# Optimization experiments

Hardware: AMD Instinct MI355X
Metric: run time of the kernel (lower is better)

The kernel has to match this reference:

```python
import jax, jax.numpy as jnp
import numpy as np

IN_FEATURES = 2048
OUT_FEATURES = 4096
NUM_SHIFTS = 10  # perms


def setup_inputs() -> dict:
    key = jax.random.key(0)
    kx, kw = jax.random.split(key)
    x = jax.random.normal(kx, (4, 2048, IN_FEATURES), dtype=jnp.float32)
    # nn.Linear weight: (out_features, in_features), Kaiming-uniform-ish init
    bound = 1.0 / np.sqrt(IN_FEATURES)
    W = jax.random.uniform(kw, (OUT_FEATURES, IN_FEATURES), dtype=jnp.float32,
                           minval=-bound, maxval=bound)
    return {"x": x, "W": W}


def _combined_weight(W):
    # Wt: (in, out). Sum of all weight variants; sum_i(x @ W_i) == x @ sum_i(W_i).
    Wt = W.T
    Weff = Wt + jnp.flip(Wt, axis=0) + jnp.flip(Wt, axis=1)
    for i in range(NUM_SHIFTS // 2):
        Weff = Weff + jnp.roll(Wt, shift=i + 1, axis=1)
        Weff = Weff + jnp.roll(Wt, shift=i + 1, axis=0)
    return Weff  # (in, out)


def reference(x, W):
    # reg_out (x @ W.T) + flipped + rolled variants, collapsed into one GEMM
    Weff = _combined_weight(W)
    return jnp.einsum('bsi,io->bso', x, Weff)
```

## Files before the change

### kernel.cpp

```cpp
#include <hip/hip_runtime.h>
#include <hip/hip_bf16.h>
#include <stdint.h>

#define M_DIM 8192
#define K_DIM 2048
#define N_DIM 4096
#define BM 256
#define BN 256
#define BK 64
#define NT (K_DIM / BK)

typedef __attribute__((ext_vector_type(8))) short bf16x8;
typedef __attribute__((ext_vector_type(4))) float f32x4;

__device__ __forceinline__ unsigned short f2bfu(float f) {
    __hip_bfloat16 h = __float2bfloat16(f);
    return __builtin_bit_cast(unsigned short, h);
}

__global__ void build_weff(const float* __restrict__ W, unsigned short* __restrict__ WT) {
    const int o = blockIdx.x;
    const float* wo  = W + (size_t)o * K_DIM;
    const float* wfo = W + (size_t)(N_DIM - 1 - o) * K_DIM;
    const float* wr0 = W + (size_t)((o - 1) & (N_DIM - 1)) * K_DIM;
    const float* wr1 = W + (size_t)((o - 2) & (N_DIM - 1)) * K_DIM;
    const float* wr2 = W + (size_t)((o - 3) & (N_DIM - 1)) * K_DIM;
    const float* wr3 = W + (size_t)((o - 4) & (N_DIM - 1)) * K_DIM;
    const float* wr4 = W + (size_t)((o - 5) & (N_DIM - 1)) * K_DIM;
    for (int i = threadIdx.x; i < K_DIM; i += 256) {
        float acc = wo[i] + wo[K_DIM - 1 - i] + wfo[i];
        acc += wo[(i - 1) & (K_DIM - 1)];
        acc += wo[(i - 2) & (K_DIM - 1)];
        acc += wo[(i - 3) & (K_DIM - 1)];
        acc += wo[(i - 4) & (K_DIM - 1)];
        acc += wo[(i - 5) & (K_DIM - 1)];
        acc += wr0[i] + wr1[i] + wr2[i] + wr3[i] + wr4[i];
        WT[(size_t)o * K_DIM + i] = f2bfu(acc);
    }
}

__global__ void cvt_x_kernel(const float* __restrict__ x, unsigned short* __restrict__ xb) {
    const int idx = blockIdx.x * 256 + threadIdx.x;
    float4 v = ((const float4*)x)[idx];
    ushort4 o;
    o.x = f2bfu(v.x); o.y = f2bfu(v.y); o.z = f2bfu(v.z); o.w = f2bfu(v.w);
    ((ushort4*)xb)[idx] = o;
}

__global__ __launch_bounds__(512, 2) void gemm256(const unsigned short* __restrict__ Ab,
                                                  const unsigned short* __restrict__ Bt,
                                                  float* __restrict__ C) {
    __shared__ __align__(16) char smem[2 * 65536];

    const int tid  = threadIdx.x;
    const int wave = tid >> 6;
    const int lane = tid & 63;

    const int nwg = gridDim.x;
    const int cpx = nwg >> 3;
    const int wg  = (blockIdx.x & 7) * cpx + (blockIdx.x >> 3);
    const int nbn = N_DIM / BN;
    const int bm0 = (wg / nbn) * BM;
    const int bn0 = (wg % nbn) * BN;

    const int wr = wave >> 2;
    const int wc = wave & 3;

    const int srow = wave * 8 + (lane >> 3);
    const int lsw  = (lane & 7) ^ ((lane >> 3) & 7);
    const unsigned short* gA0 = Ab + (size_t)(bm0 + srow) * K_DIM + lsw * 8;
    const unsigned short* gB0 = Bt + (size_t)(bn0 + srow) * K_DIM + lsw * 8;

    const int r16   = lane & 15;
    const int slot0 = (((lane >> 4) | 0) ^ (lane & 7)) * 16;
    const int slot1 = (((lane >> 4) | 4) ^ (lane & 7)) * 16;
    const int aRow  = (wr * 128 + r16) * 128;
    const int bRow  = (wc * 64  + r16) * 128;

    f32x4 acc[8][4] = {};

#define STAGE(kt, p) do {                                                          \
    char* ldsA = smem + (p) * 65536 + wave * 1024;                                 \
    char* ldsB = ldsA + 32768;                                                     \
    const unsigned short* ga = gA0 + (kt) * BK;                                    \
    const unsigned short* gb = gB0 + (kt) * BK;                                    \
    _Pragma("unroll")                                                              \
    for (int j = 0; j < 4; ++j)                                                    \
        __builtin_amdgcn_global_load_lds(                                          \
            (const __attribute__((address_space(1))) unsigned int*)(ga + (size_t)j * 64 * K_DIM), \
            (__attribute__((address_space(3))) unsigned int*)(ldsA + j * 8192),    \
            16, 0, 0);                                                             \
    _Pragma("unroll")                                                              \
    for (int j = 0; j < 4; ++j)                                                    \
        __builtin_amdgcn_global_load_lds(                                          \
            (const __attribute__((address_space(1))) unsigned int*)(gb + (size_t)j * 64 * K_DIM), \
            (__attribute__((address_space(3))) unsigned int*)(ldsB + j * 8192),    \
            16, 0, 0);                                                             \
} while (0)

    STAGE(0, 0);
    STAGE(1, 1);

    for (int k = 0; k < NT; ++k) {
        const int p = k & 1;

        if (k + 1 < NT) asm volatile("s_waitcnt vmcnt(8)" ::: "memory");
        else            asm volatile("s_waitcnt vmcnt(0)" ::: "memory");
        __builtin_amdgcn_s_barrier();
        __builtin_amdgcn_sched_barrier(0);

        const char* bufA = smem + p * 65536;
        const char* bufB = bufA + 32768;

        bf16x8 b[4][2];
#pragma unroll
        for (int fn = 0; fn < 4; ++fn) {
            b[fn][0] = *(const bf16x8*)(bufB + bRow + fn * (16 * 128) + slot0);
            b[fn][1] = *(const bf16x8*)(bufB + bRow + fn * (16 * 128) + slot1);
        }
#pragma unroll
        for (int qm = 0; qm < 2; ++qm) {
            bf16x8 a[4][2];
#pragma unroll
            for (int fm = 0; fm < 4; ++fm) {
                a[fm][0] = *(const bf16x8*)(bufA + aRow + (qm * 64 + fm * 16) * 128 + slot0);
                a[fm][1] = *(const bf16x8*)(bufA + aRow + (qm * 64 + fm * 16) * 128 + slot1);
            }
            __builtin_amdgcn_s_setprio(1);
#pragma unroll
            for (int fm = 0; fm < 4; ++fm)
#pragma unroll
                for (int fn = 0; fn < 4; ++fn) {
                    acc[qm * 4 + fm][fn] = __builtin_amdgcn_mfma_f32_16x16x32_bf16(
                        a[fm][0], b[fn][0], acc[qm * 4 + fm][fn], 0, 0, 0);
                    acc[qm * 4 + fm][fn] = __builtin_amdgcn_mfma_f32_16x16x32_bf16(
                        a[fm][1], b[fn][1], acc[qm * 4 + fm][fn], 0, 0, 0);
                }
            __builtin_amdgcn_s_setprio(0);
        }

        asm volatile("s_waitcnt lgkmcnt(0)" ::: "memory");
        __builtin_amdgcn_sched_barrier(0);
        __builtin_amdgcn_s_barrier();
        __builtin_amdgcn_sched_barrier(0);

        if (k + 2 < NT) STAGE(k + 2, p);
    }
#undef STAGE

    const int crow = (lane >> 4) * 4;
    const int ccol = lane & 15;
    float* Cb = C + (size_t)(bm0 + wr * 128 + crow) * N_DIM + (bn0 + wc * 64 + ccol);
#pragma unroll
    for (int fm = 0; fm < 8; ++fm)
#pragma unroll
        for (int fn = 0; fn < 4; ++fn)
#pragma unroll
            for (int r = 0; r < 4; ++r)
                Cb[(size_t)(fm * 16 + r) * N_DIM + fn * 16] = acc[fm][fn][r];
}

extern "C" void kernel_launch(void* const* d_in, const int* in_sizes, int n_in,
                              void* d_out, int out_size, void* d_ws, size_t ws_size,
                              hipStream_t stream) {
    const float* x = (const float*)d_in[0];
    const float* W = (const float*)d_in[1];
    float* out = (float*)d_out;

    unsigned short* xb = (unsigned short*)d_ws;
    unsigned short* wt = (unsigned short*)((char*)d_ws + (size_t)M_DIM * K_DIM * 2);

    build_weff<<<N_DIM, 256, 0, stream>>>(W, wt);
    cvt_x_kernel<<<(M_DIM * K_DIM) / 4 / 256, 256, 0, stream>>>(x, xb);

    dim3 grid((M_DIM / BM) * (N_DIM / BN));
    gemm256<<<grid, 512, 0, stream>>>(xb, wt, out);
}
```

Before: 186.7 us.

## Split GEMM main loop into eight-phase ping-pong schedule with half-tile prefetch

```diff
diff --git a/kernel.cpp b/kernel.cpp
--- a/kernel.cpp
+++ b/kernel.cpp
@@ -9,6 +9,7 @@
 #define BN 256
 #define BK 64
 #define NT (K_DIM / BK)
+#define NITER (NT / 2)
 
 typedef __attribute__((ext_vector_type(8))) short bf16x8;
 typedef __attribute__((ext_vector_type(4))) float f32x4;
@@ -47,9 +48,9 @@
     ((ushort4*)xb)[idx] = o;
 }
 
-__global__ __launch_bounds__(512, 2) void gemm256(const unsigned short* __restrict__ Ab,
-                                                  const unsigned short* __restrict__ Bt,
-                                                  float* __restrict__ C) {
+__global__ __launch_bounds__(512, 2) void gemm8p(const unsigned short* __restrict__ Ab,
+                                                 const unsigned short* __restrict__ Bt,
+                                                 float* __restrict__ C) {
     __shared__ __align__(16) char smem[2 * 65536];
 
     const int tid  = threadIdx.x;
@@ -66,87 +67,92 @@
     const int wr = wave >> 2;
     const int wc = wave & 3;
 
-    const int srow = wave * 8 + (lane >> 3);
+    const int srow = tid >> 3;
     const int lsw  = (lane & 7) ^ ((lane >> 3) & 7);
     const unsigned short* gA0 = Ab + (size_t)(bm0 + srow) * K_DIM + lsw * 8;
     const unsigned short* gB0 = Bt + (size_t)(bn0 + srow) * K_DIM + lsw * 8;
 
-    const int r16   = lane & 15;
-    const int slot0 = (((lane >> 4) | 0) ^ (lane & 7)) * 16;
-    const int slot1 = (((lane >> 4) | 4) ^ (lane & 7)) * 16;
-    const int aRow  = (wr * 128 + r16) * 128;
-    const int bRow  = (wc * 64  + r16) * 128;
+    const int r16  = lane & 15;
+    const int x7   = lane & 7;
+    const int ksl0 = (((lane >> 4)    ) ^ x7) * 16;
+    const int ksl1 = (((lane >> 4) | 4) ^ x7) * 16;
+    const int aRow = (wr * 128 + r16) * 128;
+    const int bRow = (wc * 64  + r16) * 128 + 32768;
 
-    f32x4 acc[8][4] = {};
+    f32x4  acc[8][4] = {};
+    bf16x8 b[4][2];
 
-#define STAGE(kt, p) do {                                                          \
-    char* ldsA = smem + (p) * 65536 + wave * 1024;                                 \
-    char* ldsB = ldsA + 32768;                                                     \
-    const unsigned short* ga = gA0 + (kt) * BK;                                    \
-    const unsigned short* gb = gB0 + (kt) * BK;                                    \
-    _Pragma("unroll")                                                              \
-    for (int j = 0; j < 4; ++j)                                                    \
-        __builtin_amdgcn_global_load_lds(                                          \
-            (const __attribute__((address_space(1))) unsigned int*)(ga + (size_t)j * 64 * K_DIM), \
-            (__attribute__((address_space(3))) unsigned int*)(ldsA + j * 8192),    \
-            16, 0, 0);                                                             \
-    _Pragma("unroll")                                                              \
-    for (int j = 0; j < 4; ++j)                                                    \
-        __builtin_amdgcn_global_load_lds(                                          \
-            (const __attribute__((address_space(1))) unsigned int*)(gb + (size_t)j * 64 * K_DIM), \
-            (__attribute__((address_space(3))) unsigned int*)(ldsB + j * 8192),    \
-            16, 0, 0);                                                             \
+#define STAGE_HALF(gbase, opoff, h, t, p) do {                                              \
+    char* lds_ = smem + (p) * 65536 + (opoff) + (h) * 16384 + wave * 1024;                  \
+    const unsigned short* g_ = (gbase) + (size_t)((h) * 128) * K_DIM + (t) * BK;            \
+    __builtin_amdgcn_global_load_lds(                                                        \
+        (const __attribute__((address_space(1))) unsigned int*)g_,                           \
+        (__attribute__((address_space(3))) unsigned int*)lds_, 16, 0, 0);                    \
+    __builtin_amdgcn_global_load_lds(                                                        \
+        (const __attribute__((address_space(1))) unsigned int*)(g_ + (size_t)64 * K_DIM),    \
+        (__attribute__((address_space(3))) unsigned int*)(lds_ + 8192), 16, 0, 0);           \
 } while (0)
 
-    STAGE(0, 0);
-    STAGE(1, 1);
+#define PHASE(P, Q, LOADB, STAGE_STMT, VM_STMT) do {                                        \
+    const char* base_ = smem + (P) * 65536;                                                 \
+    bf16x8 a_[2][2];                                                                        \
+    if (LOADB) {                                                                            \
+        _Pragma("unroll")                                                                   \
+        for (int fn = 0; fn < 4; ++fn) {                                                    \
+            b[fn][0] = *(const bf16x8*)(base_ + bRow + fn * 2048 + ksl0);                   \
+            b[fn][1] = *(const bf16x8*)(base_ + bRow + fn * 2048 + ksl1);                   \
+        }                                                                                   \
+    }                                                                                       \
+    a_[0][0] = *(const bf16x8*)(base_ + aRow + (Q) * 4096 + ksl0);                          \
+    a_[0][1] = *(const bf16x8*)(base_ + aRow + (Q) * 4096 + ksl1);                          \
+    a_[1][0] = *(const bf16x8*)(base_ + aRow + (Q) * 4096 + 2048 + ksl0);                   \
+    a_[1][1] = *(const bf16x8*)(base_ + aRow + (Q) * 4096 + 2048 + ksl1);                   \
+    STAGE_STMT;                                                                             \
+    __builtin_amdgcn_s_barrier();                                                           \
+    asm volatile("s_waitcnt lgkmcnt(0)" ::: "memory");                                      \
+    __builtin_amdgcn_sched_barrier(0);                                                      \
+    __builtin_amdgcn_s_setprio(1);                                                          \
+    _Pragma("unroll")                                                                       \
+    for (int fm = 0; fm < 2; ++fm)                                                          \
+        _Pragma("unroll")                                                                   \
+        for (int fn = 0; fn < 4; ++fn) {                                                    \
+            acc[(Q)*2 + fm][fn] = __builtin_amdgcn_mfma_f32_16x16x32_bf16(                  \
+                a_[fm][0], b[fn][0], acc[(Q)*2 + fm][fn], 0, 0, 0);                         \
+            acc[(Q)*2 + fm][fn] = __builtin_amdgcn_mfma_f32_16x16x32_bf16(                  \
+                a_[fm][1], b[fn][1], acc[(Q)*2 + fm][fn], 0, 0, 0);                         \
+        }                                                                                   \
+    __builtin_amdgcn_s_setprio(0);                                                          \
+    VM_STMT;                                                                                \
+    __builtin_amdgcn_s_barrier();                                                           \
+} while (0)
 
-    for (int k = 0; k < NT; ++k) {
-        const int p = k & 1;
+    STAGE_HALF(gA0, 0,     0, 0, 0);
+    STAGE_HALF(gA0, 0,     1, 0, 0);
+    STAGE_HALF(gB0, 32768, 0, 0, 0);
+    STAGE_HALF(gB0, 32768, 1, 0, 0);
+    STAGE_HALF(gB0, 32768, 0, 1, 1);
+    STAGE_HALF(gB0, 32768, 1, 1, 1);
+    asm volatile("s_waitcnt vmcnt(4)" ::: "memory");
+    __builtin_amdgcn_s_barrier();
 
-        if (k + 1 < NT) asm volatile("s_waitcnt vmcnt(8)" ::: "memory");
-        else            asm volatile("s_waitcnt vmcnt(0)" ::: "memory");
-        __builtin_amdgcn_s_barrier();
-        __builtin_amdgcn_sched_barrier(0);
+    for (int u = 0; u < NITER; ++u) {
+        const bool last = (u == NITER - 1);
+        const int  t1 = 2 * u + 1, t2 = 2 * u + 2, t3 = 2 * u + 3;
 
-        const char* bufA = smem + p * 65536;
-        const char* bufB = bufA + 32768;
-
-        bf16x8 b[4][2];
-#pragma unroll
-        for (int fn = 0; fn < 4; ++fn) {
-            b[fn][0] = *(const bf16x8*)(bufB + bRow + fn * (16 * 128) + slot0);
-            b[fn][1] = *(const bf16x8*)(bufB + bRow + fn * (16 * 128) + slot1);
-        }
-#pragma unroll
-        for (int qm = 0; qm < 2; ++qm) {
-            bf16x8 a[4][2];
-#pragma unroll
-            for (int fm = 0; fm < 4; ++fm) {
-                a[fm][0] = *(const bf16x8*)(bufA + aRow + (qm * 64 + fm * 16) * 128 + slot0);
-                a[fm][1] = *(const bf16x8*)(bufA + aRow + (qm * 64 + fm * 16) * 128 + slot1);
-            }
-            __builtin_amdgcn_s_setprio(1);
-#pragma unroll
-            for (int fm = 0; fm < 4; ++fm)
-#pragma unroll
-                for (int fn = 0; fn < 4; ++fn) {
-                    acc[qm * 4 + fm][fn] = __builtin_amdgcn_mfma_f32_16x16x32_bf16(
-                        a[fm][0], b[fn][0], acc[qm * 4 + fm][fn], 0, 0, 0);
-                    acc[qm * 4 + fm][fn] = __builtin_amdgcn_mfma_f32_16x16x32_bf16(
-                        a[fm][1], b[fn][1], acc[qm * 4 + fm][fn], 0, 0, 0);
-                }
-            __builtin_amdgcn_s_setprio(0);
-        }
-
-        asm volatile("s_waitcnt lgkmcnt(0)" ::: "memory");
-        __builtin_amdgcn_sched_barrier(0);
-        __builtin_amdgcn_s_barrier();
-        __builtin_amdgcn_sched_barrier(0);
-
-        if (k + 2 < NT) STAGE(k + 2, p);
+        PHASE(0, 0, 1, { STAGE_HALF(gA0, 0, 0, t1, 1); }, {});
+        PHASE(0, 1, 0, { STAGE_HALF(gA0, 0, 1, t1, 1); }, {});
+        PHASE(0, 2, 0, { if (!last) STAGE_HALF(gB0, 32768, 0, t2, 0); }, {});
+        PHASE(0, 3, 0, { if (!last) STAGE_HALF(gB0, 32768, 1, t2, 0); },
+              { if (last) asm volatile("s_waitcnt vmcnt(0)" ::: "memory");
+                else      asm volatile("s_waitcnt vmcnt(4)" ::: "memory"); });
+        PHASE(1, 0, 1, { if (!last) STAGE_HALF(gA0, 0, 0, t2, 0); }, {});
+        PHASE(1, 1, 0, { if (!last) STAGE_HALF(gA0, 0, 1, t2, 0); }, {});
+        PHASE(1, 2, 0, { if (!last) STAGE_HALF(gB0, 32768, 0, t3, 1); }, {});
+        PHASE(1, 3, 0, { if (!last) STAGE_HALF(gB0, 32768, 1, t3, 1); },
+              { if (!last) asm volatile("s_waitcnt vmcnt(4)" ::: "memory"); });
     }
-#undef STAGE
+#undef PHASE
+#undef STAGE_HALF
 
     const int crow = (lane >> 4) * 4;
     const int ccol = lane & 15;
@@ -174,5 +180,5 @@
     cvt_x_kernel<<<(M_DIM * K_DIM) / 4 / 256, 256, 0, stream>>>(x, xb);
 
     dim3 grid((M_DIM / BM) * (N_DIM / BN));
-    gemm256<<<grid, 512, 0, stream>>>(xb, wt, out);
+    gemm8p<<<grid, 512, 0, stream>>>(xb, wt, out);
 }
```

Result: faster. 179.9 us (-3.6%).
